# Kernel optimization log

Measured on AMD Instinct MI355X. Metric: run time of the kernel, lower is better.

Reference implementation:

```python
import math
import jax, jax.numpy as jnp
import numpy as np

B, S, D, H, DFF, BASE = 2, 2048, 1024, 16, 4096, 10000.0
HD = D // H  # 64


def setup_inputs() -> dict:
    key = jax.random.key(0)
    ks = jax.random.split(key, 16)
    sc = 0.02
    inp = {
        "x": jax.random.normal(ks[0], (B, S, D), jnp.float32),
        "positions": jnp.arange(S, dtype=jnp.int32),
        "wq": jax.random.normal(ks[1], (D, D), jnp.float32) * sc,
        "bq": jnp.zeros((D,), jnp.float32),
        "wk": jax.random.normal(ks[2], (D, D), jnp.float32) * sc,
        "bk": jnp.zeros((D,), jnp.float32),
        "wv": jax.random.normal(ks[3], (D, D), jnp.float32) * sc,
        "bv": jnp.zeros((D,), jnp.float32),
        "wo": jax.random.normal(ks[4], (D, D), jnp.float32) * sc,
        "bo": jnp.zeros((D,), jnp.float32),
        "phase_bias": jax.random.uniform(ks[5], (H, HD), jnp.float32, -2.0 * math.pi, 0.0),
        "w1": jax.random.normal(ks[6], (D, DFF), jnp.float32) * sc,
        "b1": jnp.zeros((DFF,), jnp.float32),
        "w2": jax.random.normal(ks[7], (DFF, D), jnp.float32) * sc,
        "b2": jnp.zeros((D,), jnp.float32),
        "g1": jnp.ones((D,), jnp.float32),
        "be1": jnp.zeros((D,), jnp.float32),
        "g2": jnp.ones((D,), jnp.float32),
        "be2": jnp.zeros((D,), jnp.float32),
    }
    return inp


def _layernorm(x, g, b):
    mu = jnp.mean(x, -1, keepdims=True)
    var = jnp.mean(jnp.square(x - mu), -1, keepdims=True)
    return (x - mu) / jnp.sqrt(var + 1e-5) * g + b


def _block(x, positions, wq, bq, wk, bk, wv, bv, wo, bo, phase_bias,
           w1, b1, w2, b2, g1, be1, g2, be2):
    # projections -> (B, H, S, HD)
    def heads(w, b):
        return (x @ w + b).reshape(B, S, H, HD).transpose(0, 2, 1, 3)
    q, k, v = heads(wq, bq), heads(wk, bk), heads(wv, bv)

    # PoPE: magnitudes via softplus, phases from position*freq (+ clamped bias for k)
    mu_q = jax.nn.softplus(q)
    mu_k = jax.nn.softplus(k)
    freqs = 1.0 / BASE ** (jnp.arange(HD, dtype=jnp.float32) / HD)      # (HD,)
    pos_ph = positions[:, None].astype(jnp.float32) * freqs[None, :]     # (S, HD)
    q_ph = pos_ph[None, None]                                            # (1,1,S,HD)
    cb = jnp.clip(phase_bias, -2.0 * math.pi, 0.0)
    k_ph = pos_ph[None, None] + cb[None, :, None, :]                     # (1,H,S,HD)
    q_p = jnp.concatenate([mu_q * jnp.cos(q_ph), mu_q * jnp.sin(q_ph)], -1)  # (B,H,S,2HD)
    k_p = jnp.concatenate([mu_k * jnp.cos(k_ph), mu_k * jnp.sin(k_ph)], -1)

    # manual attention with causal mask and softmax1
    scale = 1.0 / math.sqrt(2 * HD)
    scores = jnp.einsum("bhqd,bhkd->bhqk", q_p, k_p) * scale
    causal = jnp.triu(jnp.ones((S, S), bool), 1)
    scores = jnp.where(causal, -jnp.inf, scores)
    m = jnp.max(scores, -1, keepdims=True)  # finite: diagonal always unmasked
    e = jnp.exp(scores - m)
    w = e / (jnp.exp(-m) + jnp.sum(e, -1, keepdims=True))
    attn = jnp.einsum("bhqk,bhkd->bhqd", w, v)
    attn = attn.transpose(0, 2, 1, 3).reshape(B, S, D) @ wo + bo

    h = _layernorm(x + attn, g1, be1)
    ff = jax.nn.relu(h @ w1 + b1) @ w2 + b2
    return _layernorm(h + ff, g2, be2)


def reference(x, positions, wq, bq, wk, bk, wv, bv, wo, bo, phase_bias,
              w1, b1, w2, b2, g1, be1, g2, be2):
    return _block(x, positions, wq, bq, wk, bk, wv, bv, wo, bo, phase_bias,
                  w1, b1, w2, b2, g1, be1, g2, be2)
```

## Files before the change

kernel.cpp:

```cpp
#include <hip/hip_runtime.h>
#include <hip/hip_bf16.h>
#include <math.h>

#define NB 2
#define NS 2048
#define ND 1024
#define NH 16
#define NHD 64
#define NDFF 4096

typedef __attribute__((ext_vector_type(4))) float f32x4;
typedef __attribute__((ext_vector_type(8))) short bf16x8;

__device__ __forceinline__ short f2bf(float f) {
  union { float f; unsigned u; } v; v.f = f;
  unsigned r = v.u + 0x7fffu + ((v.u >> 16) & 1u);
  return (short)(r >> 16);
}
__device__ __forceinline__ float bf2f(unsigned short u) {
  union { unsigned u; float f; } v; v.u = ((unsigned)u) << 16; return v.f;
}
__device__ __forceinline__ float softplus_f(float x) {
  return fmaxf(x, 0.f) + log1pf(__expf(-fabsf(x)));
}
__device__ __forceinline__ void gl16(const short* g, short* l) {
  __builtin_amdgcn_global_load_lds(
      (const __attribute__((address_space(1))) void*)g,
      (__attribute__((address_space(3))) void*)l, 16, 0, 0);
}
__device__ __forceinline__ void xcd_map(int& row0, int& col0) {
  const int gx = gridDim.x, gy = gridDim.y;
  const int bid = blockIdx.y * gx + blockIdx.x;
  const int rows_px = gy >> 3;
  const int xcd = bid & 7, l = bid >> 3;
  row0 = (xcd * rows_px + (l % rows_px)) * 128;
  col0 = (l / rows_px) * 128;
}

__global__ __launch_bounds__(256) void k_prep(
    const float* __restrict__ wq, const float* __restrict__ wk,
    const float* __restrict__ wv, const float* __restrict__ wo,
    const float* __restrict__ w1, const float* __restrict__ w2,
    const float* __restrict__ x,
    short* __restrict__ wqT, short* __restrict__ wkT, short* __restrict__ wvT,
    short* __restrict__ woT, short* __restrict__ w1T, short* __restrict__ w2T,
    short* __restrict__ xb) {
  __shared__ float t[64][65];
  const int bid = blockIdx.x;
  if (bid >= 3072) {
    const int i = (bid - 3072) * 256 + threadIdx.x;
    const float4 a = ((const float4*)x)[i * 2];
    const float4 b = ((const float4*)x)[i * 2 + 1];
    short tmp[8] = { f2bf(a.x), f2bf(a.y), f2bf(a.z), f2bf(a.w),
                     f2bf(b.x), f2bf(b.y), f2bf(b.z), f2bf(b.w) };
    *(int4*)&xb[(size_t)i * 8] = *(const int4*)tmp;
    return;
  }
  const float* W; short* Wt; int K, N, local;
  if (bid < 1024) {
    const int wsel = bid >> 8; local = bid & 255;
    W  = wsel == 0 ? wq  : wsel == 1 ? wk  : wsel == 2 ? wv  : wo;
    Wt = wsel == 0 ? wqT : wsel == 1 ? wkT : wsel == 2 ? wvT : woT;
    K = ND; N = ND;
  } else if (bid < 2048) {
    local = bid - 1024; W = w1; Wt = w1T; K = ND; N = NDFF;
  } else {
    local = bid - 2048; W = w2; Wt = w2T; K = NDFF; N = ND;
  }
  const int nx = N >> 6;
  const int n0 = (local % nx) * 64, k0 = (local / nx) * 64;
  for (int i = threadIdx.x; i < 4096; i += 256) {
    const int r = i >> 6, c = i & 63;
    t[r][c] = W[(size_t)(k0 + r) * N + n0 + c];
  }
  __syncthreads();
  for (int i = threadIdx.x; i < 4096; i += 256) {
    const int r = i >> 6, c = i & 63;
    Wt[(size_t)(n0 + r) * K + k0 + c] = f2bf(t[c][r]);
  }
}

__global__ __launch_bounds__(256) void k_pope_pv(const short* __restrict__ qb,
    const short* __restrict__ kb, const short* __restrict__ vb,
    const int* __restrict__ positions, const float* __restrict__ phb,
    short* __restrict__ qp, short* __restrict__ kp, short* __restrict__ vt) {
  __shared__ short t[64][72];
  const int bid = blockIdx.x;
  if (bid < 2048) {
    const size_t i8 = ((size_t)bid * 256 + threadIdx.x) * 8;
    const int d0 = (int)(i8 & 63);
    const int h  = (int)((i8 >> 6) & 15);
    const int s  = (int)((i8 >> 10) & 2047);
    const int b  = (int)(i8 >> 21);
    const float posf = (float)positions[s];
    const float QSC = 0.12751743305610407f;
    int4 qv = *(const int4*)&qb[i8];
    int4 kv = *(const int4*)&kb[i8];
    const short* qs = (const short*)&qv;
    const short* ks = (const short*)&kv;
    short qc[8], qsn[8], kc[8], ksn[8];
#pragma unroll
    for (int j = 0; j < 8; j++) {
      const int d = d0 + j;
      const float freq = __expf(-(float)d * (float)(9.210340371976184 / 64.0));
      const float muq = softplus_f(bf2f((unsigned short)qs[j])) * QSC;
      const float muk = softplus_f(bf2f((unsigned short)ks[j]));
      float cb = phb[h * 64 + d];
      cb = fminf(fmaxf(cb, -6.283185307179586f), 0.f);
      float snq, csq, snk, csk;
      __sincosf(posf * freq, &snq, &csq);
      __sincosf(posf * freq + cb, &snk, &csk);
      qc[j] = f2bf(muq * csq); qsn[j] = f2bf(muq * snq);
      kc[j] = f2bf(muk * csk); ksn[j] = f2bf(muk * snk);
    }
    const size_t o = (((size_t)(b * 16 + h) * NS + s) * 128) + d0;
    *(int4*)&qp[o] = *(const int4*)qc;
    *(int4*)&qp[o + 64] = *(const int4*)qsn;
    *(int4*)&kp[o] = *(const int4*)kc;
    *(int4*)&kp[o + 64] = *(const int4*)ksn;
  } else {
    const int local = bid - 2048;
    const int bh = local >> 5, b = bh >> 4, h = bh & 15;
    const int s0 = (local & 31) * 64;
    for (int i = threadIdx.x; i < 512; i += 256) {
      const int sl = i >> 3, d8 = (i & 7) * 8;
      int4 vv = *(const int4*)&vb[((size_t)(b * NS + s0 + sl) * NH + h) * NHD + d8];
      const short* sp = (const short*)&vv;
#pragma unroll
      for (int j = 0; j < 8; j++) t[d8 + j][sl] = sp[j];
    }
    __syncthreads();
    for (int i = threadIdx.x; i < 512; i += 256) {
      const int d = i >> 3, c8 = (i & 7) * 8;
      *(int4*)&vt[((size_t)bh * 64 + d) * NS + s0 + c8] = *(const int4*)&t[d][c8];
    }
  }
}

#define BKK 32

__device__ __forceinline__ void gemm_core(const short* __restrict__ A,
    const short* __restrict__ Wt, const int K, const int kbeg, const int kend,
    const int row0, const int col0, short* lsA, short* lsB, f32x4 acc[4][4]) {
  const int tid = threadIdx.x;
  const int lane = tid & 63, wave = tid >> 6;
  const int lr = lane & 15, lk8 = (lane >> 4) << 3;
  const int wr = wave >> 1, wc = wave & 1;
  const int srow = lane >> 2, scol = (lane & 3) << 3;
  const int wbase = wave * 32;
#pragma unroll
  for (int m = 0; m < 4; m++)
#pragma unroll
    for (int n = 0; n < 4; n++) acc[m][n] = 0.f;
  const short* gA0 = &A[(size_t)(row0 + wbase + srow) * K + scol];
  const short* gA1 = gA0 + (size_t)16 * K;
  const short* gB0 = &Wt[(size_t)(col0 + wbase + srow) * K + scol];
  const short* gB1 = gB0 + (size_t)16 * K;
  short* const lA0 = lsA + wbase * 32;
  short* const lB0 = lsB + wbase * 32;
  auto stage = [&](int buf, int kk) {
    const int o = buf * 4096;
    gl16(gA0 + kk, lA0 + o);
    gl16(gA1 + kk, lA0 + o + 512);
    gl16(gB0 + kk, lB0 + o);
    gl16(gB1 + kk, lB0 + o + 512);
  };
  stage(0, kbeg);
  __syncthreads();
  int cur = 0;
  for (int k0 = kbeg; k0 < kend; k0 += BKK) {
    if (k0 + BKK < kend) stage(cur ^ 1, k0 + BKK);
    const short* la = lsA + cur * 4096;
    const short* lb = lsB + cur * 4096;
    bf16x8 af[4], bf_[4];
#pragma unroll
    for (int m = 0; m < 4; m++)
      af[m] = *(const bf16x8*)&la[(wr * 64 + m * 16 + lr) * 32 + lk8];
#pragma unroll
    for (int n = 0; n < 4; n++)
      bf_[n] = *(const bf16x8*)&lb[(wc * 64 + n * 16 + lr) * 32 + lk8];
#pragma unroll
    for (int m = 0; m < 4; m++)
#pragma unroll
      for (int n = 0; n < 4; n++)
        acc[m][n] = __builtin_amdgcn_mfma_f32_16x16x32_bf16(af[m], bf_[n], acc[m][n], 0, 0, 0);
    __syncthreads();
    cur ^= 1;
  }
}

template<int RELU, int OUTBF16>
__global__ __launch_bounds__(256) void k_gemm(const short* __restrict__ A,
    const short* __restrict__ Wt, const float* __restrict__ bias,
    void* __restrict__ C, int M, int N, int K) {
  __shared__ short lsA[2 * 4096], lsB[2 * 4096];
  f32x4 acc[4][4];
  int row0, col0;
  xcd_map(row0, col0);
  gemm_core(A, Wt, K, 0, K, row0, col0, lsA, lsB, acc);
  const int lane = threadIdx.x & 63, wave = threadIdx.x >> 6;
  const int lr = lane & 15, r4 = (lane >> 4) << 2;
  const int wr = wave >> 1, wc = wave & 1;
#pragma unroll
  for (int m = 0; m < 4; m++) {
#pragma unroll
    for (int n = 0; n < 4; n++) {
      const int col = col0 + wc * 64 + n * 16 + lr;
      const float bv = bias[col];
#pragma unroll
      for (int r = 0; r < 4; r++) {
        const int row = row0 + wr * 64 + m * 16 + r4 + r;
        float val = acc[m][n][r] + bv;
        if (RELU) val = fmaxf(val, 0.f);
        if (OUTBF16) ((short*)C)[(size_t)row * N + col] = f2bf(val);
        else ((float*)C)[(size_t)row * N + col] = val;
      }
    }
  }
}

__global__ __launch_bounds__(256) void k_gemm3(const short* __restrict__ xb,
    const short* __restrict__ wqT, const short* __restrict__ wkT,
    const short* __restrict__ wvT, const float* __restrict__ bq,
    const float* __restrict__ bk, const float* __restrict__ bv,
    short* __restrict__ qb, short* __restrict__ kb, short* __restrict__ vb) {
  __shared__ short lsA[2 * 4096], lsB[2 * 4096];
  const int z = blockIdx.z;
  const short* Wt = (z == 0) ? wqT : (z == 1) ? wkT : wvT;
  const float* bias = (z == 0) ? bq : (z == 1) ? bk : bv;
  short* C = (z == 0) ? qb : (z == 1) ? kb : vb;
  f32x4 acc[4][4];
  int row0, col0;
  xcd_map(row0, col0);
  gemm_core(xb, Wt, ND, 0, ND, row0, col0, lsA, lsB, acc);
  const int lane = threadIdx.x & 63, wave = threadIdx.x >> 6;
  const int lr = lane & 15, r4 = (lane >> 4) << 2;
  const int wr = wave >> 1, wc = wave & 1;
#pragma unroll
  for (int m = 0; m < 4; m++) {
#pragma unroll
    for (int n = 0; n < 4; n++) {
      const int col = col0 + wc * 64 + n * 16 + lr;
      const float bvs = bias[col];
#pragma unroll
      for (int r = 0; r < 4; r++) {
        const int row = row0 + wr * 64 + m * 16 + r4 + r;
        C[(size_t)row * ND + col] = f2bf(acc[m][n][r] + bvs);
      }
    }
  }
}

__global__ __launch_bounds__(256) void k_gemm_sk(const short* __restrict__ A,
    const short* __restrict__ Wt, float* __restrict__ C0, float* __restrict__ C1,
    int M, int N, int K) {
  __shared__ short lsA[2 * 4096], lsB[2 * 4096];
  f32x4 acc[4][4];
  const int z = blockIdx.z;
  const int khalf = K >> 1, kbeg = z * khalf, kend = kbeg + khalf;
  int row0, col0;
  xcd_map(row0, col0);
  gemm_core(A, Wt, K, kbeg, kend, row0, col0, lsA, lsB, acc);
  float* C = z ? C1 : C0;
  const int lane = threadIdx.x & 63, wave = threadIdx.x >> 6;
  const int lr = lane & 15, r4 = (lane >> 4) << 2;
  const int wr = wave >> 1, wc = wave & 1;
#pragma unroll
  for (int m = 0; m < 4; m++) {
#pragma unroll
    for (int n = 0; n < 4; n++) {
      const int col = col0 + wc * 64 + n * 16 + lr;
#pragma unroll
      for (int r = 0; r < 4; r++) {
        const int row = row0 + wr * 64 + m * 16 + r4 + r;
        C[(size_t)row * N + col] = acc[m][n][r];
      }
    }
  }
}

__device__ __forceinline__ void attn_proc(const bf16x8 aq[4], f32x4 acc_o[4],
    float l_p[4], const int rowb, const int kb,
    const short (*kpl)[136], const short (*vl)[72], short (*pl)[72],
    const int lr, const int lk) {
  f32x4 s_acc[4];
#pragma unroll
  for (int n = 0; n < 4; n++) s_acc[n] = 0.f;
#pragma unroll
  for (int ks = 0; ks < 4; ks++) {
    bf16x8 bk_[4];
#pragma unroll
    for (int n = 0; n < 4; n++)
      bk_[n] = *(const bf16x8*)&kpl[n * 16 + lr][ks * 32 + lk * 8];
#pragma unroll
    for (int n = 0; n < 4; n++)
      s_acc[n] = __builtin_amdgcn_mfma_f32_16x16x32_bf16(aq[ks], bk_[n], s_acc[n], 0, 0, 0);
  }
  const bool domask = (kb + 63 > rowb);
#pragma unroll
  for (int n = 0; n < 4; n++) {
#pragma unroll
    for (int r = 0; r < 4; r++) {
      float p = __builtin_amdgcn_exp2f(s_acc[n][r]);
      if (domask) {
        const int rel = rowb + lk * 4 + r - kb;
        p = (n * 16 + lr <= rel) ? p : 0.f;
      }
      unsigned pu = __float_as_uint(p) & 0xFFFF0000u;
      l_p[r] += __uint_as_float(pu);
      pl[lk * 4 + r][n * 16 + lr] = (short)(pu >> 16);
    }
  }
#pragma unroll
  for (int ks = 0; ks < 2; ks++) {
    const bf16x8 ap = *(const bf16x8*)&pl[lr][ks * 32 + lk * 8];
    bf16x8 bv_[4];
#pragma unroll
    for (int nd = 0; nd < 4; nd++)
      bv_[nd] = *(const bf16x8*)&vl[nd * 16 + lr][ks * 32 + lk * 8];
#pragma unroll
    for (int nd = 0; nd < 4; nd++)
      acc_o[nd] = __builtin_amdgcn_mfma_f32_16x16x32_bf16(ap, bv_[nd], acc_o[nd], 0, 0, 0);
  }
}

__global__ __launch_bounds__(512) void k_attn3(
    const short* __restrict__ qp, const short* __restrict__ kp,
    const short* __restrict__ vt, short* __restrict__ attn) {
  __shared__ short kp_l[2][64][136];
  __shared__ short v_l[2][64][72];
  __shared__ short p_l[8][16][72];
  const int bid = blockIdx.y * gridDim.x + blockIdx.x;
  const int xcd = bid & 7, o = bid >> 3;
  const int bh = xcd * 4 + (o >> 4);
  const int bx = o & 15;
  const int b = bh >> 4, h = bh & 15;
  const int tid = threadIdx.x, wave = tid >> 6, lane = tid & 63;
  const int lr = lane & 15, lk = lane >> 4;
  const int tHeavy = 31 - bx;
  const int myTile = (wave < 4) ? tHeavy : bx;
  const int rowb = myTile * 64 + (wave & 3) * 16;
  const int nch = tHeavy + 1;

  bf16x8 aq[4];
  {
    const short* qrow = qp + ((size_t)bh * NS + rowb + lr) * 128;
#pragma unroll
    for (int ks = 0; ks < 4; ks++)
      aq[ks] = *(const bf16x8*)&qrow[ks * 32 + lk * 8];
  }
  f32x4 acc[4];
  float lsum[4];
#pragma unroll
  for (int r = 0; r < 4; r++) lsum[r] = 0.f;
#pragma unroll
  for (int n = 0; n < 4; n++) acc[n] = 0.f;

  const short* kpb = kp + (size_t)bh * NS * 128;
  const short* vtb = vt + (size_t)bh * 64 * NS;
  const int krow = tid >> 3, kcol = (tid & 7) * 16;
  const int vrow = tid >> 3, vcol = (tid & 7) * 8;

  int4 rk0, rk1, rv;
  {
    const short* s = &kpb[(size_t)krow * 128 + kcol];
    rk0 = ((const int4*)s)[0]; rk1 = ((const int4*)s)[1];
    rv = *(const int4*)&vtb[(size_t)vrow * NS + vcol];
  }
  ((int4*)&kp_l[0][krow][kcol])[0] = rk0;
  ((int4*)&kp_l[0][krow][kcol])[1] = rk1;
  *(int4*)&v_l[0][vrow][vcol] = rv;
  __syncthreads();

  for (int c = 0; c < nch; c++) {
    const int kb = c * 64;
    const int cur = c & 1;
    const bool more = (c + 1) < nch;
    if (more) {
      const int kb2 = kb + 64;
      const short* s = &kpb[(size_t)(kb2 + krow) * 128 + kcol];
      rk0 = ((const int4*)s)[0]; rk1 = ((const int4*)s)[1];
      rv = *(const int4*)&vtb[(size_t)vrow * NS + kb2 + vcol];
    }
    if (rowb + 15 >= kb)
      attn_proc(aq, acc, lsum, rowb, kb, kp_l[cur], v_l[cur], p_l[wave], lr, lk);
    if (more) {
      ((int4*)&kp_l[cur ^ 1][krow][kcol])[0] = rk0;
      ((int4*)&kp_l[cur ^ 1][krow][kcol])[1] = rk1;
      *(int4*)&v_l[cur ^ 1][vrow][vcol] = rv;
    }
    __syncthreads();
  }
#pragma unroll
  for (int r = 0; r < 4; r++) {
    float s = lsum[r];
#pragma unroll
    for (int off = 8; off; off >>= 1) s += __shfl_xor(s, off);
    lsum[r] = 1.f / (1.f + s);
  }
#pragma unroll
  for (int nd = 0; nd < 4; nd++) {
#pragma unroll
    for (int r = 0; r < 4; r++) {
      const int d = nd * 16 + lr;
      const int row = rowb + lk * 4 + r;
      attn[(((size_t)b * NS + row) * NH + h) * NHD + d] = f2bf(acc[nd][r] * lsum[r]);
    }
  }
}

template<int RBF16, int OUTBF16>
__global__ __launch_bounds__(256) void k_ln3(const float* __restrict__ A0,
    const float* __restrict__ A1, const float* __restrict__ badd,
    const void* __restrict__ Rv, const float* __restrict__ g,
    const float* __restrict__ be, void* __restrict__ out) {
  const int row = blockIdx.x, tid = threadIdx.x;
  const float4 a0 = ((const float4*)(A0 + (size_t)row * ND))[tid];
  const float4 a1 = ((const float4*)(A1 + (size_t)row * ND))[tid];
  const float4 bd = ((const float4*)badd)[tid];
  float r0, r1, r2, r3;
  if (RBF16) {
    short4 rr = *(const short4*)((const short*)Rv + (size_t)row * ND + tid * 4);
    r0 = bf2f((unsigned short)rr.x); r1 = bf2f((unsigned short)rr.y);
    r2 = bf2f((unsigned short)rr.z); r3 = bf2f((unsigned short)rr.w);
  } else {
    const float4 rr = ((const float4*)((const float*)Rv + (size_t)row * ND))[tid];
    r0 = rr.x; r1 = rr.y; r2 = rr.z; r3 = rr.w;
  }
  const float x0 = a0.x + a1.x + bd.x + r0;
  const float x1 = a0.y + a1.y + bd.y + r1;
  const float x2 = a0.z + a1.z + bd.z + r2;
  const float x3 = a0.w + a1.w + bd.w + r3;
  float s = x0 + x1 + x2 + x3;
  float sq = x0 * x0 + x1 * x1 + x2 * x2 + x3 * x3;
#pragma unroll
  for (int off = 32; off; off >>= 1) {
    s += __shfl_xor(s, off);
    sq += __shfl_xor(sq, off);
  }
  __shared__ float ss[4], ssq[4];
  const int wave = tid >> 6, lane = tid & 63;
  if (lane == 0) { ss[wave] = s; ssq[wave] = sq; }
  __syncthreads();
  s = ss[0] + ss[1] + ss[2] + ss[3];
  sq = ssq[0] + ssq[1] + ssq[2] + ssq[3];
  const float mu = s * (1.f / (float)ND);
  const float var = sq * (1.f / (float)ND) - mu * mu;
  const float rstd = rsqrtf(var + 1e-5f);
  const float4 gg = ((const float4*)g)[tid];
  const float4 bb = ((const float4*)be)[tid];
  const float o0 = (x0 - mu) * rstd * gg.x + bb.x;
  const float o1 = (x1 - mu) * rstd * gg.y + bb.y;
  const float o2 = (x2 - mu) * rstd * gg.z + bb.z;
  const float o3 = (x3 - mu) * rstd * gg.w + bb.w;
  if (OUTBF16) {
    short4 ov = { f2bf(o0), f2bf(o1), f2bf(o2), f2bf(o3) };
    *(short4*)((short*)out + (size_t)row * ND + tid * 4) = ov;
  } else {
    float4 ov = { o0, o1, o2, o3 };
    ((float4*)((float*)out + (size_t)row * ND))[tid] = ov;
  }
}

extern "C" void kernel_launch(void* const* d_in, const int* in_sizes, int n_in,
                              void* d_out, int out_size, void* d_ws, size_t ws_size,
                              hipStream_t stream) {
  const float* x   = (const float*)d_in[0];
  const int*   pos = (const int*)d_in[1];
  const float* wq  = (const float*)d_in[2];
  const float* bq  = (const float*)d_in[3];
  const float* wk  = (const float*)d_in[4];
  const float* bk  = (const float*)d_in[5];
  const float* wv  = (const float*)d_in[6];
  const float* bv  = (const float*)d_in[7];
  const float* wo  = (const float*)d_in[8];
  const float* bo  = (const float*)d_in[9];
  const float* phb = (const float*)d_in[10];
  const float* w1  = (const float*)d_in[11];
  const float* b1  = (const float*)d_in[12];
  const float* w2  = (const float*)d_in[13];
  const float* b2  = (const float*)d_in[14];
  const float* g1  = (const float*)d_in[15];
  const float* be1 = (const float*)d_in[16];
  const float* g2  = (const float*)d_in[17];
  const float* be2 = (const float*)d_in[18];

  char* ws = (char*)d_ws;
  const size_t MB = 1024 * 1024;
  if (ws_size < 112 * MB) return;
  short* qb     = (short*)(ws + 0 * MB);
  short* kb     = (short*)(ws + 8 * MB);
  short* vb     = (short*)(ws + 16 * MB);
  short* qp     = (short*)(ws + 24 * MB);
  short* kp     = (short*)(ws + 40 * MB);
  short* vt     = (short*)(ws + 56 * MB);
  short* xb     = (short*)(ws + 64 * MB);
  short* attnb  = (short*)(ws + 72 * MB);
  float* attnC0 = (float*)(ws + 0 * MB);
  float* attnC1 = (float*)(ws + 24 * MB);
  short* hb     = (short*)(ws + 16 * MB);
  short* ffh    = (short*)(ws + 40 * MB);
  float* ffC0   = (float*)(ws + 72 * MB);
  float* ffC1   = (float*)(ws + 0 * MB);
  short* wqT    = (short*)(ws + 88 * MB);
  short* wkT    = (short*)(ws + 90 * MB);
  short* wvT    = (short*)(ws + 92 * MB);
  short* woT    = (short*)(ws + 94 * MB);
  short* w1T    = (short*)(ws + 96 * MB);
  short* w2T    = (short*)(ws + 104 * MB);

  dim3 blk(256);
  k_prep<<<dim3(5120), blk, 0, stream>>>(wq, wk, wv, wo, w1, w2, x,
                                         wqT, wkT, wvT, woT, w1T, w2T, xb);
  k_gemm3<<<dim3(ND / 128, (NB * NS) / 128, 3), blk, 0, stream>>>(
      xb, wqT, wkT, wvT, bq, bk, bv, qb, kb, vb);
  k_pope_pv<<<dim3(3072), blk, 0, stream>>>(qb, kb, vb, pos, phb, qp, kp, vt);
  k_attn3<<<dim3(16, NB * NH), dim3(512), 0, stream>>>(qp, kp, vt, attnb);
  k_gemm_sk<<<dim3(ND / 128, (NB * NS) / 128, 2), blk, 0, stream>>>(
      attnb, woT, attnC0, attnC1, NB * NS, ND, ND);
  k_ln3<0, 1><<<dim3(NB * NS), blk, 0, stream>>>(attnC0, attnC1, bo, x, g1, be1, hb);
  k_gemm<1, 1><<<dim3(NDFF / 128, (NB * NS) / 128), blk, 0, stream>>>(
      hb, w1T, b1, ffh, NB * NS, NDFF, ND);
  k_gemm_sk<<<dim3(ND / 128, (NB * NS) / 128, 2), blk, 0, stream>>>(
      ffh, w2T, ffC0, ffC1, NB * NS, ND, NDFF);
  k_ln3<1, 0><<<dim3(NB * NS), blk, 0, stream>>>(ffC0, ffC1, b2, hb, g2, be2, (float*)d_out);
}
```

Baseline: 265.7 us.

## Process two 16-row query tiles per wave in attention to reuse K/V fragments

The attention kernel now gives each wave 32 query rows (two 16-row sub-tiles) instead of 16, and halves the block to 256 threads. Each K fragment loaded from LDS feeds MFMAs for both sub-tiles, and V fragments are loaded once and shared across both PV products, which cuts LDS read traffic per MFMA. Global-to-LDS staging per thread doubles. The trade-off is higher register pressure and fewer waves per block, which may reduce latency hiding. A causal skip flag avoids computing the upper sub-tile where it is fully masked.

```diff
diff --git a/kernel.cpp b/kernel.cpp
--- a/kernel.cpp
+++ b/kernel.cpp
@@ -279,13 +279,15 @@
   }
 }
 
-__device__ __forceinline__ void attn_proc(const bf16x8 aq[4], f32x4 acc_o[4],
-    float l_p[4], const int rowb, const int kb,
+__device__ __forceinline__ void attn_proc2(
+    const bf16x8 aq0[4], const bf16x8 aq1[4],
+    f32x4 acc0[4], f32x4 acc1[4], float l0[4], float l1[4],
+    const int rowb, const int kb, const bool live0,
     const short (*kpl)[136], const short (*vl)[72], short (*pl)[72],
     const int lr, const int lk) {
-  f32x4 s_acc[4];
-#pragma unroll
-  for (int n = 0; n < 4; n++) s_acc[n] = 0.f;
+  f32x4 s0[4], s1[4];
+#pragma unroll
+  for (int n = 0; n < 4; n++) { s0[n] = 0.f; s1[n] = 0.f; }
 #pragma unroll
   for (int ks = 0; ks < 4; ks++) {
     bf16x8 bk_[4];
@@ -294,42 +296,76 @@
       bk_[n] = *(const bf16x8*)&kpl[n * 16 + lr][ks * 32 + lk * 8];
 #pragma unroll
     for (int n = 0; n < 4; n++)
-      s_acc[n] = __builtin_amdgcn_mfma_f32_16x16x32_bf16(aq[ks], bk_[n], s_acc[n], 0, 0, 0);
-  }
-  const bool domask = (kb + 63 > rowb);
-#pragma unroll
-  for (int n = 0; n < 4; n++) {
-#pragma unroll
-    for (int r = 0; r < 4; r++) {
-      float p = __builtin_amdgcn_exp2f(s_acc[n][r]);
-      if (domask) {
-        const int rel = rowb + lk * 4 + r - kb;
-        p = (n * 16 + lr <= rel) ? p : 0.f;
+      s1[n] = __builtin_amdgcn_mfma_f32_16x16x32_bf16(aq1[ks], bk_[n], s1[n], 0, 0, 0);
+    if (live0) {
+#pragma unroll
+      for (int n = 0; n < 4; n++)
+        s0[n] = __builtin_amdgcn_mfma_f32_16x16x32_bf16(aq0[ks], bk_[n], s0[n], 0, 0, 0);
+    }
+  }
+  bf16x8 vf[2][4];
+#pragma unroll
+  for (int ks = 0; ks < 2; ks++)
+#pragma unroll
+    for (int nd = 0; nd < 4; nd++)
+      vf[ks][nd] = *(const bf16x8*)&vl[nd * 16 + lr][ks * 32 + lk * 8];
+  {
+    const int rb1 = rowb + 16;
+    const bool domask = (kb + 63 > rb1);
+#pragma unroll
+    for (int n = 0; n < 4; n++) {
+#pragma unroll
+      for (int r = 0; r < 4; r++) {
+        float p = __builtin_amdgcn_exp2f(s1[n][r]);
+        if (domask) {
+          const int rel = rb1 + lk * 4 + r - kb;
+          p = (n * 16 + lr <= rel) ? p : 0.f;
+        }
+        unsigned pu = __float_as_uint(p) & 0xFFFF0000u;
+        l1[r] += __uint_as_float(pu);
+        pl[lk * 4 + r][n * 16 + lr] = (short)(pu >> 16);
       }
-      unsigned pu = __float_as_uint(p) & 0xFFFF0000u;
-      l_p[r] += __uint_as_float(pu);
-      pl[lk * 4 + r][n * 16 + lr] = (short)(pu >> 16);
-    }
-  }
-#pragma unroll
-  for (int ks = 0; ks < 2; ks++) {
-    const bf16x8 ap = *(const bf16x8*)&pl[lr][ks * 32 + lk * 8];
-    bf16x8 bv_[4];
-#pragma unroll
-    for (int nd = 0; nd < 4; nd++)
-      bv_[nd] = *(const bf16x8*)&vl[nd * 16 + lr][ks * 32 + lk * 8];
-#pragma unroll
-    for (int nd = 0; nd < 4; nd++)
-      acc_o[nd] = __builtin_amdgcn_mfma_f32_16x16x32_bf16(ap, bv_[nd], acc_o[nd], 0, 0, 0);
-  }
-}
-
-__global__ __launch_bounds__(512) void k_attn3(
+    }
+#pragma unroll
+    for (int ks = 0; ks < 2; ks++) {
+      const bf16x8 ap = *(const bf16x8*)&pl[lr][ks * 32 + lk * 8];
+#pragma unroll
+      for (int nd = 0; nd < 4; nd++)
+        acc1[nd] = __builtin_amdgcn_mfma_f32_16x16x32_bf16(ap, vf[ks][nd], acc1[nd], 0, 0, 0);
+    }
+  }
+  if (live0) {
+    const bool domask = (kb + 63 > rowb);
+#pragma unroll
+    for (int n = 0; n < 4; n++) {
+#pragma unroll
+      for (int r = 0; r < 4; r++) {
+        float p = __builtin_amdgcn_exp2f(s0[n][r]);
+        if (domask) {
+          const int rel = rowb + lk * 4 + r - kb;
+          p = (n * 16 + lr <= rel) ? p : 0.f;
+        }
+        unsigned pu = __float_as_uint(p) & 0xFFFF0000u;
+        l0[r] += __uint_as_float(pu);
+        pl[lk * 4 + r][n * 16 + lr] = (short)(pu >> 16);
+      }
+    }
+#pragma unroll
+    for (int ks = 0; ks < 2; ks++) {
+      const bf16x8 ap = *(const bf16x8*)&pl[lr][ks * 32 + lk * 8];
+#pragma unroll
+      for (int nd = 0; nd < 4; nd++)
+        acc0[nd] = __builtin_amdgcn_mfma_f32_16x16x32_bf16(ap, vf[ks][nd], acc0[nd], 0, 0, 0);
+    }
+  }
+}
+
+__global__ __launch_bounds__(256) void k_attn4(
     const short* __restrict__ qp, const short* __restrict__ kp,
     const short* __restrict__ vt, short* __restrict__ attn) {
   __shared__ short kp_l[2][64][136];
   __shared__ short v_l[2][64][72];
-  __shared__ short p_l[8][16][72];
+  __shared__ short p_l[4][16][72];
   const int bid = blockIdx.y * gridDim.x + blockIdx.x;
   const int xcd = bid & 7, o = bid >> 3;
   const int bh = xcd * 4 + (o >> 4);
@@ -338,38 +374,44 @@
   const int tid = threadIdx.x, wave = tid >> 6, lane = tid & 63;
   const int lr = lane & 15, lk = lane >> 4;
   const int tHeavy = 31 - bx;
-  const int myTile = (wave < 4) ? tHeavy : bx;
-  const int rowb = myTile * 64 + (wave & 3) * 16;
+  const int myTile = (wave < 2) ? tHeavy : bx;
+  const int rowb = myTile * 64 + (wave & 1) * 32;
   const int nch = tHeavy + 1;
 
-  bf16x8 aq[4];
+  bf16x8 aq0[4], aq1[4];
   {
-    const short* qrow = qp + ((size_t)bh * NS + rowb + lr) * 128;
-#pragma unroll
-    for (int ks = 0; ks < 4; ks++)
-      aq[ks] = *(const bf16x8*)&qrow[ks * 32 + lk * 8];
-  }
-  f32x4 acc[4];
-  float lsum[4];
-#pragma unroll
-  for (int r = 0; r < 4; r++) lsum[r] = 0.f;
-#pragma unroll
-  for (int n = 0; n < 4; n++) acc[n] = 0.f;
+    const short* q0 = qp + ((size_t)bh * NS + rowb + lr) * 128;
+    const short* q1 = q0 + 16 * 128;
+#pragma unroll
+    for (int ks = 0; ks < 4; ks++) {
+      aq0[ks] = *(const bf16x8*)&q0[ks * 32 + lk * 8];
+      aq1[ks] = *(const bf16x8*)&q1[ks * 32 + lk * 8];
+    }
+  }
+  f32x4 acc0[4], acc1[4];
+  float l0[4], l1[4];
+#pragma unroll
+  for (int r = 0; r < 4; r++) { l0[r] = 0.f; l1[r] = 0.f; }
+#pragma unroll
+  for (int n = 0; n < 4; n++) { acc0[n] = 0.f; acc1[n] = 0.f; }
 
   const short* kpb = kp + (size_t)bh * NS * 128;
   const short* vtb = vt + (size_t)bh * 64 * NS;
-  const int krow = tid >> 3, kcol = (tid & 7) * 16;
-  const int vrow = tid >> 3, vcol = (tid & 7) * 8;
-
-  int4 rk0, rk1, rv;
+  const int krow = tid >> 2, kcol = (tid & 3) * 32;
+  const int vrow = tid >> 2, vcol = (tid & 3) * 16;
+
+  int4 rk[4], rv[2];
   {
     const short* s = &kpb[(size_t)krow * 128 + kcol];
-    rk0 = ((const int4*)s)[0]; rk1 = ((const int4*)s)[1];
-    rv = *(const int4*)&vtb[(size_t)vrow * NS + vcol];
-  }
-  ((int4*)&kp_l[0][krow][kcol])[0] = rk0;
-  ((int4*)&kp_l[0][krow][kcol])[1] = rk1;
-  *(int4*)&v_l[0][vrow][vcol] = rv;
+#pragma unroll
+    for (int i = 0; i < 4; i++) rk[i] = ((const int4*)s)[i];
+    const short* v = &vtb[(size_t)vrow * NS + vcol];
+    rv[0] = ((const int4*)v)[0]; rv[1] = ((const int4*)v)[1];
+  }
+#pragma unroll
+  for (int i = 0; i < 4; i++) ((int4*)&kp_l[0][krow][kcol])[i] = rk[i];
+  ((int4*)&v_l[0][vrow][vcol])[0] = rv[0];
+  ((int4*)&v_l[0][vrow][vcol])[1] = rv[1];
   __syncthreads();
 
   for (int c = 0; c < nch; c++) {
@@ -379,32 +421,42 @@
     if (more) {
       const int kb2 = kb + 64;
       const short* s = &kpb[(size_t)(kb2 + krow) * 128 + kcol];
-      rk0 = ((const int4*)s)[0]; rk1 = ((const int4*)s)[1];
-      rv = *(const int4*)&vtb[(size_t)vrow * NS + kb2 + vcol];
-    }
-    if (rowb + 15 >= kb)
-      attn_proc(aq, acc, lsum, rowb, kb, kp_l[cur], v_l[cur], p_l[wave], lr, lk);
+#pragma unroll
+      for (int i = 0; i < 4; i++) rk[i] = ((const int4*)s)[i];
+      const short* v = &vtb[(size_t)vrow * NS + kb2 + vcol];
+      rv[0] = ((const int4*)v)[0]; rv[1] = ((const int4*)v)[1];
+    }
+    if (rowb + 31 >= kb)
+      attn_proc2(aq0, aq1, acc0, acc1, l0, l1, rowb, kb, rowb + 15 >= kb,
+                 kp_l[cur], v_l[cur], p_l[wave], lr, lk);
     if (more) {
-      ((int4*)&kp_l[cur ^ 1][krow][kcol])[0] = rk0;
-      ((int4*)&kp_l[cur ^ 1][krow][kcol])[1] = rk1;
-      *(int4*)&v_l[cur ^ 1][vrow][vcol] = rv;
+#pragma unroll
+      for (int i = 0; i < 4; i++) ((int4*)&kp_l[cur ^ 1][krow][kcol])[i] = rk[i];
+      ((int4*)&v_l[cur ^ 1][vrow][vcol])[0] = rv[0];
+      ((int4*)&v_l[cur ^ 1][vrow][vcol])[1] = rv[1];
     }
     __syncthreads();
   }
 #pragma unroll
   for (int r = 0; r < 4; r++) {
-    float s = lsum[r];
-#pragma unroll
-    for (int off = 8; off; off >>= 1) s += __shfl_xor(s, off);
-    lsum[r] = 1.f / (1.f + s);
+    float s0 = l0[r], s1 = l1[r];
+#pragma unroll
+    for (int off = 8; off; off >>= 1) {
+      s0 += __shfl_xor(s0, off);
+      s1 += __shfl_xor(s1, off);
+    }
+    l0[r] = 1.f / (1.f + s0);
+    l1[r] = 1.f / (1.f + s1);
   }
 #pragma unroll
   for (int nd = 0; nd < 4; nd++) {
 #pragma unroll
     for (int r = 0; r < 4; r++) {
       const int d = nd * 16 + lr;
-      const int row = rowb + lk * 4 + r;
-      attn[(((size_t)b * NS + row) * NH + h) * NHD + d] = f2bf(acc[nd][r] * lsum[r]);
+      const int row0i = rowb + lk * 4 + r;
+      const int row1i = rowb + 16 + lk * 4 + r;
+      attn[(((size_t)b * NS + row0i) * NH + h) * NHD + d] = f2bf(acc0[nd][r] * l0[r]);
+      attn[(((size_t)b * NS + row1i) * NH + h) * NHD + d] = f2bf(acc1[nd][r] * l1[r]);
     }
   }
 }
@@ -515,7 +567,7 @@
   k_gemm3<<<dim3(ND / 128, (NB * NS) / 128, 3), blk, 0, stream>>>(
       xb, wqT, wkT, wvT, bq, bk, bv, qb, kb, vb);
   k_pope_pv<<<dim3(3072), blk, 0, stream>>>(qb, kb, vb, pos, phb, qp, kp, vt);
-  k_attn3<<<dim3(16, NB * NH), dim3(512), 0, stream>>>(qp, kp, vt, attnb);
+  k_attn4<<<dim3(16, NB * NH), dim3(256), 0, stream>>>(qp, kp, vt, attnb);
   k_gemm_sk<<<dim3(ND / 128, (NB * NS) / 128, 2), blk, 0, stream>>>(
       attnb, woT, attnC0, attnC1, NB * NS, ND, ND);
   k_ln3<0, 1><<<dim3(NB * NS), blk, 0, stream>>>(attnC0, attnC1, bo, x, g1, be1, hb);
```

Result: slower. 319.2 us (+20.2%).
